# Kernel tuning notes

Hardware: AMD Instinct MI355X
Metric: run time of the kernel (lower is better)

## Reference

```python
import jax, jax.numpy as jnp
import numpy as np

N = 100000
E = 1600000
C_IN = 32
C_OUT = 64
B = 4
VOXEL_SIZE = 0.0625
GRID_LO, GRID_HI = 0.0, 1.0
VOX = int((GRID_HI - GRID_LO) / VOXEL_SIZE)  # 16
R_CORR = GRID_HI - GRID_LO  # r_correction = max(grid_scale) - min(grid_scale) = 1


def setup_inputs() -> dict:
    key = jax.random.key(0)
    k1, k2, k3, k4, k5, k6 = jax.random.split(key, 6)
    x = jax.random.normal(k1, (N, C_IN), dtype=jnp.float32)
    edge_index = jax.random.randint(k2, (2, E), 0, N, dtype=jnp.int32)
    pos = jax.random.uniform(k3, (N, 2), dtype=jnp.float32)
    batch = jnp.sort(jax.random.randint(k4, (N,), 0, B, dtype=jnp.int32))
    W = jax.random.normal(k5, (C_OUT, 4 * C_IN), dtype=jnp.float32) / np.sqrt(4 * C_IN)
    b = jax.random.normal(k6, (C_OUT,), dtype=jnp.float32) * 0.01
    return {"x": x, "edge_index": edge_index, "pos": pos, "batch": batch, "W": W, "b": b}


def dpo_conv(x, edge_index, pos, W, b):
    row, col = edge_index[0], edge_index[1]  # j = source, i = target (PyG default flow)
    pos_i, pos_j = pos[col], pos[row]        # [E, 2]
    v_i, v_j = x[col], x[row]                # [E, C_IN]
    diff = pos_i - pos_j                     # [E, 2]
    r2 = jnp.sum(diff * diff, axis=1, keepdims=True)  # [E, 1]
    w = diff * R_CORR / (r2 + 0.01)          # [E, 2] -> columns are diff_x, diff_y
    v_diff = v_i - v_j                       # [E, C_IN]
    # message f: [E, 3*C_IN]
    f = jnp.concatenate([v_diff * w[:, 0:1], v_diff * w[:, 1:2], v_j], axis=1)
    # scatter-mean into target nodes i = col
    summed = jax.ops.segment_sum(f, col, num_segments=N)            # [N, 3*C_IN]
    cnt = jax.ops.segment_sum(jnp.ones((E, 1), f.dtype), col, num_segments=N)
    prop = summed / jnp.maximum(cnt, 1.0)
    prop = jnp.concatenate([prop, x], axis=1)  # [N, 4*C_IN]
    return prop @ W.T + b


def reference(x, edge_index, pos, batch, W, b):
    h = jax.nn.relu(dpo_conv(x, edge_index, pos, W, b))  # [N, C_OUT]
    # voxel_grid: per-graph voxel cluster ids, then max_pool per cluster (dense grid)
    vox = jnp.clip(jnp.floor((pos - GRID_LO) / VOXEL_SIZE).astype(jnp.int32), 0, VOX - 1)
    cluster = batch * (VOX * VOX) + vox[:, 1] * VOX + vox[:, 0]     # [N]
    n_clusters = B * VOX * VOX
    pooled_x = jax.ops.segment_max(h, cluster, num_segments=n_clusters)  # [B*V^2, C_OUT]
    pooled_x = jnp.where(jnp.isfinite(pooled_x), pooled_x, 0.0)          # empty voxels -> 0
    pos_sum = jax.ops.segment_sum(pos, cluster, num_segments=n_clusters)
    node_cnt = jax.ops.segment_sum(jnp.ones((N, 1), pos.dtype), cluster, num_segments=n_clusters)
    pooled_pos = pos_sum / jnp.maximum(node_cnt, 1.0)                    # mean pos per voxel
    return pooled_x, pooled_pos, pos, batch
```

## Files before the change

### kernel.cpp

```cpp
#include <hip/hip_runtime.h>
#include <hip/hip_fp16.h>

#define NN 100000
#define NE 1600000
#define NCLUST 1024
#define OUT_POOLED_POS 65536
#define OUT_POS        67584
#define OUT_BATCH      267584

static __device__ __forceinline__ float2 h2f(unsigned int u)
{
    __half2 h = *reinterpret_cast<__half2*>(&u);
    return __half22float2(h);
}

__global__ __launch_bounds__(256) void cvt_kernel(const float4* __restrict__ x4,
                                                  uint2* __restrict__ xh2)
{
    int t = blockIdx.x * 256 + threadIdx.x;
    if (t >= NN * 8) return;
    float4 v = x4[t];
    __half2 lo = __floats2half2_rn(v.x, v.y);
    __half2 hi = __floats2half2_rn(v.z, v.w);
    uint2 o;
    o.x = *reinterpret_cast<unsigned int*>(&lo);
    o.y = *reinterpret_cast<unsigned int*>(&hi);
    xh2[t] = o;
}

__global__ __launch_bounds__(256) void fill_kernel(const int* __restrict__ ei,
                                                   const float2* __restrict__ pos2,
                                                   int* __restrict__ wp,
                                                   uint2* __restrict__ csr64,
                                                   int cap)
{
    int t = blockIdx.x * 256 + threadIdx.x;
    int e0 = t * 4;
    if (e0 + 3 < NE) {
        int4 r = *(const int4*)(ei + e0);
        int4 c = *(const int4*)(ei + NE + e0);
        int rr[4] = {r.x, r.y, r.z, r.w};
        int cc[4] = {c.x, c.y, c.z, c.w};
        #pragma unroll
        for (int u = 0; u < 4; ++u) {
            int row = rr[u], col = cc[u];
            float2 pi = pos2[col], pj = pos2[row];
            float dx = pi.x - pj.x, dy = pi.y - pj.y;
            float inv = __builtin_amdgcn_rcpf(dx * dx + dy * dy + 0.01f);
            __half2 h2 = __floats2half2_rn(dx * inv, dy * inv);
            unsigned int wbits = *reinterpret_cast<unsigned int*>(&h2);
            int s = atomicAdd(&wp[col], 1);
            if (s < cap) csr64[(size_t)col * cap + s] = make_uint2((unsigned)row, wbits);
        }
    } else {
        for (int e = e0; e < NE; ++e) {
            int row = ei[e], col = ei[NE + e];
            float2 pi = pos2[col], pj = pos2[row];
            float dx = pi.x - pj.x, dy = pi.y - pj.y;
            float inv = __builtin_amdgcn_rcpf(dx * dx + dy * dy + 0.01f);
            __half2 h2 = __floats2half2_rn(dx * inv, dy * inv);
            unsigned int wbits = *reinterpret_cast<unsigned int*>(&h2);
            int s = atomicAdd(&wp[col], 1);
            if (s < cap) csr64[(size_t)col * cap + s] = make_uint2((unsigned)row, wbits);
        }
    }
}

__global__ __launch_bounds__(1024, 8) void fused_kernel(
    const float2* __restrict__ xf2,
    const unsigned int* __restrict__ xh32,
    const float2* __restrict__ pos2,
    const int* __restrict__ batch,
    const float4* __restrict__ W4,
    const float* __restrict__ bv,
    const int* __restrict__ wp,
    const uint2* __restrict__ csr64,
    int cap,
    float* __restrict__ out,
    float* __restrict__ pos_sum,
    float* __restrict__ node_cnt)
{
    __shared__ float4 Wt4[32 * 64];
    __shared__ float  bs[64];
    __shared__ float4 prop4[16][4][32];

    {
        int oc0 = threadIdx.x & 63;
        int k0  = threadIdx.x >> 6;
        Wt4[k0 * 64 + oc0]        = W4[oc0 * 32 + k0];
        Wt4[(k0 + 16) * 64 + oc0] = W4[oc0 * 32 + k0 + 16];
        if (threadIdx.x < 64) bs[threadIdx.x] = bv[threadIdx.x];
    }
    __syncthreads();

    const int wid  = threadIdx.x >> 6;
    const int lane = threadIdx.x & 63;
    const int q  = lane >> 4;
    const int s  = lane & 15;
    const int oc = lane;
    const int nwaves = gridDim.x * 16;

    for (int wg = blockIdx.x * 16 + wid; wg * 4 < NN; wg += nwaves) {
        int n = wg * 4 + q;
        bool act = (n < NN);
        int nn = act ? n : 0;

        int cnt = wp[nn];
        int deg = act ? min(cnt, cap) : 0;
        float2 vi = xf2[(size_t)nn * 16 + s];
        const uint2* bk = csr64 + (size_t)nn * cap;

        int md = deg;
        md = max(md, __shfl_xor(md, 16));
        md = max(md, __shfl_xor(md, 32));

        float a0x = 0.f, a0y = 0.f;
        float a1x = 0.f, a1y = 0.f;
        float a2x = 0.f, a2y = 0.f;

        uint2 E0 = (0 < deg) ? bk[0] : make_uint2((unsigned)nn, 0u);
        uint2 E1 = (1 < deg) ? bk[1] : make_uint2((unsigned)nn, 0u);
        uint2 E2 = (2 < deg) ? bk[2] : make_uint2((unsigned)nn, 0u);
        uint2 E3 = (3 < deg) ? bk[3] : make_uint2((unsigned)nn, 0u);
        unsigned int X0 = xh32[(size_t)E0.x * 16 + s];
        unsigned int X1 = xh32[(size_t)E1.x * 16 + s];
        unsigned int X2 = xh32[(size_t)E2.x * 16 + s];
        unsigned int X3 = xh32[(size_t)E3.x * 16 + s];
        unsigned int B0 = E0.y, B1 = E1.y, B2 = E2.y, B3 = E3.y;
        float m0 = (0 < deg) ? 1.f : 0.f;
        float m1 = (1 < deg) ? 1.f : 0.f;
        float m2 = (2 < deg) ? 1.f : 0.f;
        float m3 = (3 < deg) ? 1.f : 0.f;

        int kb = 0;
        int iters = (md + 3) >> 2;
        for (int it = 0; it < iters; ++it) {
            int nb = kb + 4;
            uint2 F0 = (nb     < deg) ? bk[nb]     : make_uint2((unsigned)nn, 0u);
            uint2 F1 = (nb + 1 < deg) ? bk[nb + 1] : make_uint2((unsigned)nn, 0u);
            uint2 F2 = (nb + 2 < deg) ? bk[nb + 2] : make_uint2((unsigned)nn, 0u);
            uint2 F3 = (nb + 3 < deg) ? bk[nb + 3] : make_uint2((unsigned)nn, 0u);

            {
                float2 w0 = h2f(B0), w1 = h2f(B1), w2 = h2f(B2), w3 = h2f(B3);
                float2 v0 = h2f(X0), v1 = h2f(X1), v2 = h2f(X2), v3 = h2f(X3);
                float vdx, vdy;
                vdx = vi.x - v0.x; vdy = vi.y - v0.y;
                a0x += vdx * w0.x; a0y += vdy * w0.x;
                a1x += vdx * w0.y; a1y += vdy * w0.y;
                a2x += v0.x * m0;  a2y += v0.y * m0;

                vdx = vi.x - v1.x; vdy = vi.y - v1.y;
                a0x += vdx * w1.x; a0y += vdy * w1.x;
                a1x += vdx * w1.y; a1y += vdy * w1.y;
                a2x += v1.x * m1;  a2y += v1.y * m1;

                vdx = vi.x - v2.x; vdy = vi.y - v2.y;
                a0x += vdx * w2.x; a0y += vdy * w2.x;
                a1x += vdx * w2.y; a1y += vdy * w2.y;
                a2x += v2.x * m2;  a2y += v2.y * m2;

                vdx = vi.x - v3.x; vdy = vi.y - v3.y;
                a0x += vdx * w3.x; a0y += vdy * w3.x;
                a1x += vdx * w3.y; a1y += vdy * w3.y;
                a2x += v3.x * m3;  a2y += v3.y * m3;
            }

            if (it + 1 < iters) {
                X0 = xh32[(size_t)F0.x * 16 + s];
                X1 = xh32[(size_t)F1.x * 16 + s];
                X2 = xh32[(size_t)F2.x * 16 + s];
                X3 = xh32[(size_t)F3.x * 16 + s];
                B0 = F0.y; B1 = F1.y; B2 = F2.y; B3 = F3.y;
                m0 = (nb     < deg) ? 1.f : 0.f;
                m1 = (nb + 1 < deg) ? 1.f : 0.f;
                m2 = (nb + 2 < deg) ? 1.f : 0.f;
                m3 = (nb + 3 < deg) ? 1.f : 0.f;
            }
            kb = nb;
        }

        float invd = 1.0f / fmaxf((float)cnt, 1.0f);
        if (act) {
            float2* pw = (float2*)&prop4[wid][q][0];
            pw[s]      = make_float2(a0x * invd, a0y * invd);
            pw[16 + s] = make_float2(a1x * invd, a1y * invd);
            pw[32 + s] = make_float2(a2x * invd, a2y * invd);
            pw[48 + s] = vi;
        }
        asm volatile("s_waitcnt lgkmcnt(0)" ::: "memory");

        float bb = bs[oc];
        float acc0 = bb, acc1 = bb, acc2 = bb, acc3 = bb;
        #pragma unroll 8
        for (int k4 = 0; k4 < 32; ++k4) {
            float4 w   = Wt4[k4 * 64 + oc];
            float4 pp0 = prop4[wid][0][k4];
            float4 pp1 = prop4[wid][1][k4];
            float4 pp2 = prop4[wid][2][k4];
            float4 pp3 = prop4[wid][3][k4];
            acc0 += w.x*pp0.x + w.y*pp0.y + w.z*pp0.z + w.w*pp0.w;
            acc1 += w.x*pp1.x + w.y*pp1.y + w.z*pp1.z + w.w*pp1.w;
            acc2 += w.x*pp2.x + w.y*pp2.y + w.z*pp2.z + w.w*pp2.w;
            acc3 += w.x*pp3.x + w.y*pp3.y + w.z*pp3.z + w.w*pp3.w;
        }

        float accq[4] = {acc0, acc1, acc2, acc3};
        #pragma unroll
        for (int qq = 0; qq < 4; ++qq) {
            int n2 = wg * 4 + qq;
            if (n2 < NN) {
                float h = fmaxf(accq[qq], 0.0f);
                float2 pp = pos2[n2];
                int b = batch[n2];
                int vx = min(max((int)floorf(pp.x * 16.0f), 0), 15);
                int vy = min(max((int)floorf(pp.y * 16.0f), 0), 15);
                int cl = b * 256 + vy * 16 + vx;
                unsigned int* tgt = (unsigned int*)(out + (size_t)cl * 64 + oc);
                unsigned int prev = *tgt;
                unsigned int cur  = __float_as_uint(h);
                if (cur > prev) atomicMax(tgt, cur);
                if (oc == qq) {
                    *(float2*)(out + OUT_POS + 2 * (size_t)n2) = pp;
                    out[OUT_BATCH + n2] = (float)b;
                    atomicAdd(pos_sum + 2 * cl,     pp.x);
                    atomicAdd(pos_sum + 2 * cl + 1, pp.y);
                    atomicAdd(node_cnt + cl, 1.0f);
                }
            }
        }
        asm volatile("s_waitcnt lgkmcnt(0)" ::: "memory");
    }
}

__global__ void finalize_kernel(const float* __restrict__ pos_sum,
                                const float* __restrict__ node_cnt,
                                float* __restrict__ out_pooled_pos)
{
    int c = blockIdx.x * blockDim.x + threadIdx.x;
    if (c >= NCLUST) return;
    float inv = 1.0f / fmaxf(node_cnt[c], 1.0f);
    out_pooled_pos[2 * c]     = pos_sum[2 * c] * inv;
    out_pooled_pos[2 * c + 1] = pos_sum[2 * c + 1] * inv;
}

extern "C" void kernel_launch(void* const* d_in, const int* in_sizes, int n_in,
                              void* d_out, int out_size, void* d_ws, size_t ws_size,
                              hipStream_t stream)
{
    const float* x     = (const float*)d_in[0];
    const int*   ei    = (const int*)d_in[1];
    const float* pos   = (const float*)d_in[2];
    const int*   batch = (const int*)d_in[3];
    const float* W     = (const float*)d_in[4];
    const float* bvec  = (const float*)d_in[5];
    float* out = (float*)d_out;

    size_t fixed = (size_t)NN * 4 + (size_t)NN * 8 * 8 + 3 * NCLUST * 4;
    int cap = 40;
    if (ws_size < fixed + (size_t)NN * cap * 8) {
        cap = (int)((ws_size - fixed) / ((size_t)NN * 8));
        if (cap > 40) cap = 40;
    }

    int* wp = (int*)d_ws;
    uint2* csr64 = (uint2*)(wp + NN);
    uint2* xh2 = csr64 + (size_t)NN * cap;
    float* pos_sum  = (float*)(xh2 + (size_t)NN * 8);
    float* node_cnt = pos_sum + 2 * NCLUST;

    hipMemsetAsync(wp, 0, NN * sizeof(int), stream);
    hipMemsetAsync(pos_sum, 0, 3 * NCLUST * sizeof(float), stream);
    hipMemsetAsync(d_out, 0, (size_t)NCLUST * 64 * sizeof(float), stream);

    cvt_kernel<<<(NN * 8 + 255) / 256, 256, 0, stream>>>((const float4*)x, xh2);

    fill_kernel<<<(NE / 4 + 255) / 256, 256, 0, stream>>>(
        ei, (const float2*)pos, wp, csr64, cap);

    fused_kernel<<<512, 1024, 0, stream>>>(
        (const float2*)x, (const unsigned int*)xh2, (const float2*)pos, batch,
        (const float4*)W, bvec, wp, csr64, cap, out, pos_sum, node_cnt);

    finalize_kernel<<<(NCLUST + 255) / 256, 256, 0, stream>>>(
        pos_sum, node_cnt, out + NCLUST * 64);
}
```

Measured before the change: 248.7 us.

## Transpose edge bucket layout slot-major and deepen gather prefetch to eight edges

The padded per-node edge buckets move from node-major (col*cap+s) to slot-major (s*NN+col), so the 4 nodes handled by a wave read adjacent slots and the fill kernel's scattered writes land in a shared slot row. The gather loop now processes 8 edges per iteration instead of 4, with deeper software prefetch. Padding entries point to an extra zeroed feature row, which removes the per-edge mask multiply. The price is more registers per lane, more wasted iterations for low-degree nodes, and one extra memset.

```diff
diff --git a/kernel.cpp b/kernel.cpp
--- a/kernel.cpp
+++ b/kernel.cpp
@@ -7,6 +7,7 @@
 #define OUT_POOLED_POS 65536
 #define OUT_POS        67584
 #define OUT_BATCH      267584
+#define ZROW ((unsigned)NN)
 
 static __device__ __forceinline__ float2 h2f(unsigned int u)
 {
@@ -50,7 +51,7 @@
             __half2 h2 = __floats2half2_rn(dx * inv, dy * inv);
             unsigned int wbits = *reinterpret_cast<unsigned int*>(&h2);
             int s = atomicAdd(&wp[col], 1);
-            if (s < cap) csr64[(size_t)col * cap + s] = make_uint2((unsigned)row, wbits);
+            if (s < cap) csr64[(size_t)s * NN + col] = make_uint2((unsigned)row, wbits);
         }
     } else {
         for (int e = e0; e < NE; ++e) {
@@ -61,7 +62,7 @@
             __half2 h2 = __floats2half2_rn(dx * inv, dy * inv);
             unsigned int wbits = *reinterpret_cast<unsigned int*>(&h2);
             int s = atomicAdd(&wp[col], 1);
-            if (s < cap) csr64[(size_t)col * cap + s] = make_uint2((unsigned)row, wbits);
+            if (s < cap) csr64[(size_t)s * NN + col] = make_uint2((unsigned)row, wbits);
         }
     }
 }
@@ -99,6 +100,7 @@
     const int s  = lane & 15;
     const int oc = lane;
     const int nwaves = gridDim.x * 16;
+    const uint2 ZE = make_uint2(ZROW, 0u);
 
     for (int wg = blockIdx.x * 16 + wid; wg * 4 < NN; wg += nwaves) {
         int n = wg * 4 + q;
@@ -108,7 +110,7 @@
         int cnt = wp[nn];
         int deg = act ? min(cnt, cap) : 0;
         float2 vi = xf2[(size_t)nn * 16 + s];
-        const uint2* bk = csr64 + (size_t)nn * cap;
+        const uint2* bkp = csr64 + nn;
 
         int md = deg;
         md = max(md, __shfl_xor(md, 16));
@@ -118,64 +120,59 @@
         float a1x = 0.f, a1y = 0.f;
         float a2x = 0.f, a2y = 0.f;
 
-        uint2 E0 = (0 < deg) ? bk[0] : make_uint2((unsigned)nn, 0u);
-        uint2 E1 = (1 < deg) ? bk[1] : make_uint2((unsigned)nn, 0u);
-        uint2 E2 = (2 < deg) ? bk[2] : make_uint2((unsigned)nn, 0u);
-        uint2 E3 = (3 < deg) ? bk[3] : make_uint2((unsigned)nn, 0u);
-        unsigned int X0 = xh32[(size_t)E0.x * 16 + s];
-        unsigned int X1 = xh32[(size_t)E1.x * 16 + s];
-        unsigned int X2 = xh32[(size_t)E2.x * 16 + s];
-        unsigned int X3 = xh32[(size_t)E3.x * 16 + s];
-        unsigned int B0 = E0.y, B1 = E1.y, B2 = E2.y, B3 = E3.y;
-        float m0 = (0 < deg) ? 1.f : 0.f;
-        float m1 = (1 < deg) ? 1.f : 0.f;
-        float m2 = (2 < deg) ? 1.f : 0.f;
-        float m3 = (3 < deg) ? 1.f : 0.f;
+        uint2 E0 = (0 < deg) ? bkp[(size_t)0 * NN] : ZE;
+        uint2 E1 = (1 < deg) ? bkp[(size_t)1 * NN] : ZE;
+        uint2 E2 = (2 < deg) ? bkp[(size_t)2 * NN] : ZE;
+        uint2 E3 = (3 < deg) ? bkp[(size_t)3 * NN] : ZE;
+        uint2 E4 = (4 < deg) ? bkp[(size_t)4 * NN] : ZE;
+        uint2 E5 = (5 < deg) ? bkp[(size_t)5 * NN] : ZE;
+        uint2 E6 = (6 < deg) ? bkp[(size_t)6 * NN] : ZE;
+        uint2 E7 = (7 < deg) ? bkp[(size_t)7 * NN] : ZE;
+        unsigned X0 = xh32[(size_t)E0.x * 16 + s];
+        unsigned X1 = xh32[(size_t)E1.x * 16 + s];
+        unsigned X2 = xh32[(size_t)E2.x * 16 + s];
+        unsigned X3 = xh32[(size_t)E3.x * 16 + s];
+        unsigned X4 = xh32[(size_t)E4.x * 16 + s];
+        unsigned X5 = xh32[(size_t)E5.x * 16 + s];
+        unsigned X6 = xh32[(size_t)E6.x * 16 + s];
+        unsigned X7 = xh32[(size_t)E7.x * 16 + s];
+        unsigned B0 = E0.y, B1 = E1.y, B2 = E2.y, B3 = E3.y;
+        unsigned B4 = E4.y, B5 = E5.y, B6 = E6.y, B7 = E7.y;
 
         int kb = 0;
-        int iters = (md + 3) >> 2;
+        int iters = (md + 7) >> 3;
         for (int it = 0; it < iters; ++it) {
-            int nb = kb + 4;
-            uint2 F0 = (nb     < deg) ? bk[nb]     : make_uint2((unsigned)nn, 0u);
-            uint2 F1 = (nb + 1 < deg) ? bk[nb + 1] : make_uint2((unsigned)nn, 0u);
-            uint2 F2 = (nb + 2 < deg) ? bk[nb + 2] : make_uint2((unsigned)nn, 0u);
-            uint2 F3 = (nb + 3 < deg) ? bk[nb + 3] : make_uint2((unsigned)nn, 0u);
-
-            {
-                float2 w0 = h2f(B0), w1 = h2f(B1), w2 = h2f(B2), w3 = h2f(B3);
-                float2 v0 = h2f(X0), v1 = h2f(X1), v2 = h2f(X2), v3 = h2f(X3);
-                float vdx, vdy;
-                vdx = vi.x - v0.x; vdy = vi.y - v0.y;
-                a0x += vdx * w0.x; a0y += vdy * w0.x;
-                a1x += vdx * w0.y; a1y += vdy * w0.y;
-                a2x += v0.x * m0;  a2y += v0.y * m0;
-
-                vdx = vi.x - v1.x; vdy = vi.y - v1.y;
-                a0x += vdx * w1.x; a0y += vdy * w1.x;
-                a1x += vdx * w1.y; a1y += vdy * w1.y;
-                a2x += v1.x * m1;  a2y += v1.y * m1;
-
-                vdx = vi.x - v2.x; vdy = vi.y - v2.y;
-                a0x += vdx * w2.x; a0y += vdy * w2.x;
-                a1x += vdx * w2.y; a1y += vdy * w2.y;
-                a2x += v2.x * m2;  a2y += v2.y * m2;
-
-                vdx = vi.x - v3.x; vdy = vi.y - v3.y;
-                a0x += vdx * w3.x; a0y += vdy * w3.x;
-                a1x += vdx * w3.y; a1y += vdy * w3.y;
-                a2x += v3.x * m3;  a2y += v3.y * m3;
+            int nb = kb + 8;
+            uint2 F0 = (nb     < deg) ? bkp[(size_t)(nb    ) * NN] : ZE;
+            uint2 F1 = (nb + 1 < deg) ? bkp[(size_t)(nb + 1) * NN] : ZE;
+            uint2 F2 = (nb + 2 < deg) ? bkp[(size_t)(nb + 2) * NN] : ZE;
+            uint2 F3 = (nb + 3 < deg) ? bkp[(size_t)(nb + 3) * NN] : ZE;
+            uint2 F4 = (nb + 4 < deg) ? bkp[(size_t)(nb + 4) * NN] : ZE;
+            uint2 F5 = (nb + 5 < deg) ? bkp[(size_t)(nb + 5) * NN] : ZE;
+            uint2 F6 = (nb + 6 < deg) ? bkp[(size_t)(nb + 6) * NN] : ZE;
+            uint2 F7 = (nb + 7 < deg) ? bkp[(size_t)(nb + 7) * NN] : ZE;
+
+            #define EDGE(Bi, Xi)                                              \
+            {                                                                 \
+                float2 w = h2f(Bi), v = h2f(Xi);                              \
+                float vdx = vi.x - v.x, vdy = vi.y - v.y;                     \
+                a0x += vdx * w.x; a0y += vdy * w.x;                           \
+                a1x += vdx * w.y; a1y += vdy * w.y;                           \
+                a2x += v.x;       a2y += v.y;                                 \
             }
+            EDGE(B0, X0) EDGE(B1, X1) EDGE(B2, X2) EDGE(B3, X3)
+            EDGE(B4, X4) EDGE(B5, X5) EDGE(B6, X6) EDGE(B7, X7)
+            #undef EDGE
 
             if (it + 1 < iters) {
-                X0 = xh32[(size_t)F0.x * 16 + s];
-                X1 = xh32[(size_t)F1.x * 16 + s];
-                X2 = xh32[(size_t)F2.x * 16 + s];
-                X3 = xh32[(size_t)F3.x * 16 + s];
-                B0 = F0.y; B1 = F1.y; B2 = F2.y; B3 = F3.y;
-                m0 = (nb     < deg) ? 1.f : 0.f;
-                m1 = (nb + 1 < deg) ? 1.f : 0.f;
-                m2 = (nb + 2 < deg) ? 1.f : 0.f;
-                m3 = (nb + 3 < deg) ? 1.f : 0.f;
+                X0 = xh32[(size_t)F0.x * 16 + s]; B0 = F0.y;
+                X1 = xh32[(size_t)F1.x * 16 + s]; B1 = F1.y;
+                X2 = xh32[(size_t)F2.x * 16 + s]; B2 = F2.y;
+                X3 = xh32[(size_t)F3.x * 16 + s]; B3 = F3.y;
+                X4 = xh32[(size_t)F4.x * 16 + s]; B4 = F4.y;
+                X5 = xh32[(size_t)F5.x * 16 + s]; B5 = F5.y;
+                X6 = xh32[(size_t)F6.x * 16 + s]; B6 = F6.y;
+                X7 = xh32[(size_t)F7.x * 16 + s]; B7 = F7.y;
             }
             kb = nb;
         }
@@ -256,7 +253,7 @@
     const float* bvec  = (const float*)d_in[5];
     float* out = (float*)d_out;
 
-    size_t fixed = (size_t)NN * 4 + (size_t)NN * 8 * 8 + 3 * NCLUST * 4;
+    size_t fixed = (size_t)NN * 4 + (size_t)(NN + 1) * 8 * 8 + 3 * NCLUST * 4;
     int cap = 40;
     if (ws_size < fixed + (size_t)NN * cap * 8) {
         cap = (int)((ws_size - fixed) / ((size_t)NN * 8));
@@ -266,10 +263,11 @@
     int* wp = (int*)d_ws;
     uint2* csr64 = (uint2*)(wp + NN);
     uint2* xh2 = csr64 + (size_t)NN * cap;
-    float* pos_sum  = (float*)(xh2 + (size_t)NN * 8);
+    float* pos_sum  = (float*)(xh2 + (size_t)(NN + 1) * 8);
     float* node_cnt = pos_sum + 2 * NCLUST;
 
     hipMemsetAsync(wp, 0, NN * sizeof(int), stream);
+    hipMemsetAsync(xh2 + (size_t)NN * 8, 0, 64, stream);
     hipMemsetAsync(pos_sum, 0, 3 * NCLUST * sizeof(float), stream);
     hipMemsetAsync(d_out, 0, (size_t)NCLUST * 64 * sizeof(float), stream);
 
```

Result: slower. 300.1 us (+20.7%).

## Stripe CSR fill by destination range to localize scattered writes

Applied to the files above, without the earlier changes.

The fill kernel now runs a 2D grid where each y-slice handles only edges whose target node falls in a 6250-node stripe. Every slice rereads the full column array, but only edges in its stripe do the atomics and CSR writes. The aim is to keep the scattered atomics and bucket writes concentrated in a cache-sized region per slice. The cost is 16 passes over the column indices plus 16x more blocks. It also drops the scalar tail path, which is safe only because NE is a multiple of 4.

```diff
diff --git a/kernel.cpp b/kernel.cpp
--- a/kernel.cpp
+++ b/kernel.cpp
@@ -7,6 +7,8 @@
 #define OUT_POOLED_POS 65536
 #define OUT_POS        67584
 #define OUT_BATCH      267584
+#define NSTRIPE 16
+#define STRIPE_W 6250
 
 static __device__ __forceinline__ float2 h2f(unsigned int u)
 {
@@ -34,27 +36,18 @@
                                                    uint2* __restrict__ csr64,
                                                    int cap)
 {
+    int lo = blockIdx.y * STRIPE_W;
+    int hi = lo + STRIPE_W;
     int t = blockIdx.x * 256 + threadIdx.x;
     int e0 = t * 4;
-    if (e0 + 3 < NE) {
-        int4 r = *(const int4*)(ei + e0);
-        int4 c = *(const int4*)(ei + NE + e0);
-        int rr[4] = {r.x, r.y, r.z, r.w};
-        int cc[4] = {c.x, c.y, c.z, c.w};
-        #pragma unroll
-        for (int u = 0; u < 4; ++u) {
-            int row = rr[u], col = cc[u];
-            float2 pi = pos2[col], pj = pos2[row];
-            float dx = pi.x - pj.x, dy = pi.y - pj.y;
-            float inv = __builtin_amdgcn_rcpf(dx * dx + dy * dy + 0.01f);
-            __half2 h2 = __floats2half2_rn(dx * inv, dy * inv);
-            unsigned int wbits = *reinterpret_cast<unsigned int*>(&h2);
-            int s = atomicAdd(&wp[col], 1);
-            if (s < cap) csr64[(size_t)col * cap + s] = make_uint2((unsigned)row, wbits);
-        }
-    } else {
-        for (int e = e0; e < NE; ++e) {
-            int row = ei[e], col = ei[NE + e];
+    if (e0 >= NE) return;
+    int4 c = *(const int4*)(ei + NE + e0);
+    int cols[4] = {c.x, c.y, c.z, c.w};
+    #pragma unroll
+    for (int u = 0; u < 4; ++u) {
+        int col = cols[u];
+        if (col >= lo && col < hi) {
+            int row = ei[e0 + u];
             float2 pi = pos2[col], pj = pos2[row];
             float dx = pi.x - pj.x, dy = pi.y - pj.y;
             float inv = __builtin_amdgcn_rcpf(dx * dx + dy * dy + 0.01f);
@@ -122,11 +115,11 @@
         uint2 E1 = (1 < deg) ? bk[1] : make_uint2((unsigned)nn, 0u);
         uint2 E2 = (2 < deg) ? bk[2] : make_uint2((unsigned)nn, 0u);
         uint2 E3 = (3 < deg) ? bk[3] : make_uint2((unsigned)nn, 0u);
-        unsigned int X0 = xh32[(size_t)E0.x * 16 + s];
-        unsigned int X1 = xh32[(size_t)E1.x * 16 + s];
-        unsigned int X2 = xh32[(size_t)E2.x * 16 + s];
-        unsigned int X3 = xh32[(size_t)E3.x * 16 + s];
-        unsigned int B0 = E0.y, B1 = E1.y, B2 = E2.y, B3 = E3.y;
+        unsigned X0 = xh32[(size_t)E0.x * 16 + s];
+        unsigned X1 = xh32[(size_t)E1.x * 16 + s];
+        unsigned X2 = xh32[(size_t)E2.x * 16 + s];
+        unsigned X3 = xh32[(size_t)E3.x * 16 + s];
+        unsigned B0 = E0.y, B1 = E1.y, B2 = E2.y, B3 = E3.y;
         float m0 = (0 < deg) ? 1.f : 0.f;
         float m1 = (1 < deg) ? 1.f : 0.f;
         float m2 = (2 < deg) ? 1.f : 0.f;
@@ -167,11 +160,10 @@
             }
 
             if (it + 1 < iters) {
-                X0 = xh32[(size_t)F0.x * 16 + s];
-                X1 = xh32[(size_t)F1.x * 16 + s];
-                X2 = xh32[(size_t)F2.x * 16 + s];
-                X3 = xh32[(size_t)F3.x * 16 + s];
-                B0 = F0.y; B1 = F1.y; B2 = F2.y; B3 = F3.y;
+                X0 = xh32[(size_t)F0.x * 16 + s]; B0 = F0.y;
+                X1 = xh32[(size_t)F1.x * 16 + s]; B1 = F1.y;
+                X2 = xh32[(size_t)F2.x * 16 + s]; B2 = F2.y;
+                X3 = xh32[(size_t)F3.x * 16 + s]; B3 = F3.y;
                 m0 = (nb     < deg) ? 1.f : 0.f;
                 m1 = (nb + 1 < deg) ? 1.f : 0.f;
                 m2 = (nb + 2 < deg) ? 1.f : 0.f;
@@ -275,7 +267,8 @@
 
     cvt_kernel<<<(NN * 8 + 255) / 256, 256, 0, stream>>>((const float4*)x, xh2);
 
-    fill_kernel<<<(NE / 4 + 255) / 256, 256, 0, stream>>>(
+    dim3 fgrid((NE / 4 + 255) / 256, NSTRIPE);
+    fill_kernel<<<fgrid, 256, 0, stream>>>(
         ei, (const float2*)pos, wp, csr64, cap);
 
     fused_kernel<<<512, 1024, 0, stream>>>(
```

Result: slower. 254.8 us (+2.4%).
